# Kernel optimization log

Hardware: AMD Instinct MI355X
Metric: run time of the kernel (lower is better)

The kernel has to match this reference:

```python
import jax, jax.numpy as jnp
import numpy as np

T, D = 1024, 2048
H, KH, HD = 16, 4, 128
E, K, I = 8, 2, 2048
EPS = 1e-5
CAP = 30.0          # attn logit softcap and router logit softcap
BASE = 10000.0      # rope theta


def setup_inputs() -> dict:
    key = jax.random.key(0)
    ks = jax.random.split(key, 8)
    s = 0.02
    return {
        "positions": jnp.arange(T, dtype=jnp.int32),
        "hidden_states": jax.random.normal(ks[0], (T, D), jnp.float32),
        "w_qkv": jax.random.normal(ks[1], (D, (H + 2 * KH) * HD), jnp.float32) * s,
        "w_o": jax.random.normal(ks[2], (H * HD, D), jnp.float32) * s,
        "w_gate": jax.random.normal(ks[3], (D, E), jnp.float32) * s,
        "w_gate_up": jax.random.normal(ks[4], (E, D, 2 * I), jnp.float32) * s,
        "w_down": jax.random.normal(ks[5], (E, I, D), jnp.float32) * s,
        "w_pre_attn": 1.0 + 0.01 * jax.random.normal(ks[6], (D,), jnp.float32),
        "w_post_attn": jnp.ones((D,), jnp.float32),
        "w_pre_moe": 1.0 + 0.01 * jax.random.normal(ks[7], (D,), jnp.float32),
        "w_post_moe": jnp.ones((D,), jnp.float32),
    }


def rmsnorm(x, w):
    v = jnp.mean(jnp.square(x), axis=-1, keepdims=True)
    return x * jax.lax.rsqrt(v + EPS) * w


def rope_neox(pos, x):
    # x: [T, nH, HD]; full-head-dim neox-style rotation
    half = HD // 2
    inv = 1.0 / (BASE ** (jnp.arange(half, dtype=jnp.float32) * 2.0 / HD))
    f = pos.astype(jnp.float32)[:, None] * inv            # [T, half]
    cos, sin = jnp.cos(f)[:, None, :], jnp.sin(f)[:, None, :]
    x1, x2 = x[..., :half], x[..., half:]
    return jnp.concatenate([x1 * cos - x2 * sin, x2 * cos + x1 * sin], axis=-1)


def attention(pos, x, w_qkv, w_o):
    qkv = x @ w_qkv
    q, k, v = jnp.split(qkv, [H * HD, (H + KH) * HD], axis=-1)
    q = rope_neox(pos, q.reshape(T, H, HD))
    k = rope_neox(pos, k.reshape(T, KH, HD))
    v = v.reshape(T, KH, HD)
    rep = H // KH                                          # GQA repeat
    k = jnp.repeat(k, rep, axis=1)
    v = jnp.repeat(v, rep, axis=1)
    s = jnp.einsum('qhd,khd->hqk', q, k) * (HD ** -0.5)
    s = CAP * jnp.tanh(s / CAP)                            # tanh logit cap
    causal = pos[:, None] >= pos[None, :]
    s = jnp.where(causal[None], s, -1e30)
    p = jax.nn.softmax(s, axis=-1)
    o = jnp.einsum('hqk,khd->qhd', p, v).reshape(T, H * HD)
    return o @ w_o


def moe(x, w_gate, w_gate_up, w_down):
    logits = x @ w_gate
    logits = CAP * jnp.tanh(logits / CAP)                  # router softcap
    probs = jax.nn.softmax(logits, axis=-1)
    topv, topi = jax.lax.top_k(probs, K)                   # no renorm (Grok1)
    comb = jnp.zeros((T, E), probs.dtype).at[jnp.arange(T)[:, None], topi].set(topv)
    gu = jnp.einsum('td,edf->etf', x, w_gate_up)           # [E,T,2I]
    g, u = jnp.split(gu, 2, axis=-1)
    act = jax.nn.gelu(g, approximate=True) * u             # GeluAndMul(tanh)
    out_e = jnp.einsum('eti,eid->etd', act, w_down)        # [E,T,D]
    return jnp.einsum('etd,te->td', out_e, comb)


def reference(positions, hidden_states, w_qkv, w_o, w_gate, w_gate_up, w_down,
              w_pre_attn, w_post_attn, w_pre_moe, w_post_moe):
    resid = hidden_states
    h = rmsnorm(hidden_states, w_pre_attn)
    a = attention(positions, h, w_qkv, w_o)
    resid = resid + rmsnorm(a, w_post_attn)                # post_attn_norm + add
    h = rmsnorm(resid, w_pre_moe)
    m = moe(h, w_gate, w_gate_up, w_down)
    return resid + rmsnorm(m, w_post_moe)
```

## Files before the change

kernel.cpp:

```cpp
#include <hip/hip_runtime.h>

#define TT 1024
#define DD 2048
#define NH 16
#define NKV 4
#define HDIM 128
#define NE 8
#define NI 2048
#define EPSF 1e-5f
#define NP 4

typedef short bf16x8 __attribute__((ext_vector_type(8)));
typedef float f32x4 __attribute__((ext_vector_type(4)));

__device__ __forceinline__ unsigned short f2bf(float x) {
  unsigned u = __float_as_uint(x);
  u += 0x7FFFu + ((u >> 16) & 1u);
  return (unsigned short)(u >> 16);
}
__device__ __forceinline__ float bf2f(unsigned short h) {
  return __uint_as_float((unsigned)h << 16);
}
__device__ __forceinline__ void split2(float a, unsigned short& h,
                                       unsigned short& l) {
  h = f2bf(a);
  l = f2bf(a - bf2f(h));
}

__device__ __forceinline__ float wave_sum(float v) {
#pragma unroll
  for (int m = 32; m >= 1; m >>= 1) v += __shfl_xor(v, m, 64);
  return v;
}
__device__ __forceinline__ float wave_max(float v) {
#pragma unroll
  for (int m = 32; m >= 1; m >>= 1) v = fmaxf(v, __shfl_xor(v, m, 64));
  return v;
}

__device__ __forceinline__ int swz4(int r) { return (r ^ (r >> 2)) & 3; }
__device__ __forceinline__ int swz8(int r) { return (r ^ (r >> 3)) & 7; }

__device__ __forceinline__ void stage32(char* dst, const unsigned short* src,
                                        int rs, int tid) {
#pragma unroll
  for (int j = 0; j < 2; ++j) {
    int idx = tid + j * 256;
    int r = idx >> 2, c = idx & 3;
    bf16x8 v = *(const bf16x8*)(src + r * rs + c * 8);
    *(bf16x8*)(dst + r * 64 + ((c ^ swz4(r)) << 4)) = v;
  }
}
__device__ __forceinline__ void ld_frag(const char* base, int wrow, int l15,
                                        int lg, bf16x8* dst) {
#pragma unroll
  for (int i = 0; i < 4; ++i) {
    int row = wrow + i * 16 + l15;
    dst[i] = *(const bf16x8*)(base + row * 64 + ((lg ^ swz4(row)) << 4));
  }
}
__device__ __forceinline__ void mm16(const bf16x8* xa, const bf16x8* xb,
                                     f32x4 (*acc)[4]) {
#pragma unroll
  for (int mi = 0; mi < 4; ++mi)
#pragma unroll
    for (int ni = 0; ni < 4; ++ni)
      acc[mi][ni] = __builtin_amdgcn_mfma_f32_16x16x32_bf16(
          xa[mi], xb[ni], acc[mi][ni], 0, 0, 0);
}

template <int MODE>
__global__ __launch_bounds__(256) void pgemm3_k(
    const unsigned short* __restrict__ Ah, const unsigned short* __restrict__ Al,
    const unsigned short* __restrict__ Bh, const unsigned short* __restrict__ Bl,
    float* __restrict__ C, int Kh, int lda, int ldb, int ldc, long czs,
    float escale, float* __restrict__ SM, float* __restrict__ SS) {
  int z = blockIdx.z;
  int m0 = blockIdx.y * 128, n0 = blockIdx.x * 128;
  int k0 = 0, kend = Kh;
  if (MODE == 0) {
    k0 = z * Kh;
    kend = k0 + Kh;
    C += (long)z * czs;
  } else if (MODE == 1) {
    if (blockIdx.x > blockIdx.y) return;
    Ah += (long)z * TT * lda;
    Al += (long)z * TT * lda;
    Bh += (long)(z >> 2) * TT * ldb;
    Bl += (long)(z >> 2) * TT * ldb;
    C += (long)z * czs;
  } else {
    int head = z >> 2, ch = z & 3;
    int limit = (blockIdx.y + 1) * 128;
    k0 = ch * 256;
    if (k0 >= limit) return;
    kend = k0 + 256 < limit ? k0 + 256 : limit;
    Ah += (long)head * TT * lda;
    Al += (long)head * TT * lda;
    Bh += (long)(head >> 2) * HDIM * ldb;
    Bl += (long)(head >> 2) * HDIM * ldb;
    C += (long)ch * czs + head * HDIM;
  }

  __shared__ __align__(16) char lds[32768];
  int tid = threadIdx.x, lane = tid & 63, wid = tid >> 6;
  int wm = (wid >> 1) * 64, wn = (wid & 1) * 64;
  int l15 = lane & 15, lg = lane >> 4;

  f32x4 acc[4][4];
#pragma unroll
  for (int i = 0; i < 4; ++i)
#pragma unroll
    for (int j = 0; j < 4; ++j) acc[i][j] = {0.f, 0.f, 0.f, 0.f};

  for (int kt = k0; kt < kend; kt += 32) {
    __syncthreads();
    stage32(lds, Ah + (long)m0 * lda + kt, lda, tid);
    stage32(lds + 8192, Al + (long)m0 * lda + kt, lda, tid);
    stage32(lds + 16384, Bh + (long)n0 * ldb + kt, ldb, tid);
    stage32(lds + 24576, Bl + (long)n0 * ldb + kt, ldb, tid);
    __syncthreads();
    bf16x8 fah[4], fal[4], fbh[4], fbl[4];
    ld_frag(lds, wm, l15, lg, fah);
    ld_frag(lds + 16384, wn, l15, lg, fbh);
    mm16(fah, fbh, acc);
    ld_frag(lds + 24576, wn, l15, lg, fbl);
    mm16(fah, fbl, acc);
    ld_frag(lds + 8192, wm, l15, lg, fal);
    mm16(fal, fbh, acc);
  }

  if (MODE == 1) {
    int bx = blockIdx.x;
    bool diag = (bx == blockIdx.y);
    float vcap[4][4][4];
#pragma unroll
    for (int mi = 0; mi < 4; ++mi)
#pragma unroll
      for (int ni = 0; ni < 4; ++ni)
#pragma unroll
        for (int rr = 0; rr < 4; ++rr) {
          float v = acc[mi][ni][rr] * escale;
          vcap[mi][ni][rr] = 30.f * tanhf(v * (1.f / 30.f));
        }
#pragma unroll
    for (int mi = 0; mi < 4; ++mi)
#pragma unroll
      for (int ni = 0; ni < 4; ++ni)
#pragma unroll
        for (int rr = 0; rr < 4; ++rr) {
          int ml = m0 + wm + mi * 16 + lg * 4 + rr;
          int col = n0 + wn + ni * 16 + l15;
          C[(long)ml * ldc + col] = vcap[mi][ni][rr];
        }
    __syncthreads();
    float* wmx = (float*)lds;
    float* wsm = (float*)(lds + 1024);
    int ch = wid & 1;
#pragma unroll
    for (int mi = 0; mi < 4; ++mi)
#pragma unroll
      for (int rr = 0; rr < 4; ++rr) {
        int wr = wm + mi * 16 + lg * 4 + rr;
        int rowg = m0 + wr;
        float mx = -1e30f;
#pragma unroll
        for (int ni = 0; ni < 4; ++ni) {
          int colg = n0 + wn + ni * 16 + l15;
          if (!diag || colg <= rowg) mx = fmaxf(mx, vcap[mi][ni][rr]);
        }
#pragma unroll
        for (int mk = 1; mk <= 8; mk <<= 1)
          mx = fmaxf(mx, __shfl_xor(mx, mk, 64));
        if (l15 == 0) wmx[ch * 128 + wr] = mx;
      }
    __syncthreads();
#pragma unroll
    for (int mi = 0; mi < 4; ++mi)
#pragma unroll
      for (int rr = 0; rr < 4; ++rr) {
        int wr = wm + mi * 16 + lg * 4 + rr;
        int rowg = m0 + wr;
        float m2 = fmaxf(wmx[wr], wmx[128 + wr]);
        float s = 0.f;
#pragma unroll
        for (int ni = 0; ni < 4; ++ni) {
          int colg = n0 + wn + ni * 16 + l15;
          if (!diag || colg <= rowg) s += expf(vcap[mi][ni][rr] - m2);
        }
#pragma unroll
        for (int mk = 1; mk <= 8; mk <<= 1) s += __shfl_xor(s, mk, 64);
        if (l15 == 0) wsm[ch * 128 + wr] = s;
      }
    __syncthreads();
    if (tid < 128) {
      float m2 = fmaxf(wmx[tid], wmx[128 + tid]);
      float s = wsm[tid] + wsm[128 + tid];
      long so = ((long)z * 8 + bx) * TT + m0 + tid;
      SM[so] = m2;
      SS[so] = s;
    }
    return;
  }

#pragma unroll
  for (int mi = 0; mi < 4; ++mi)
#pragma unroll
    for (int ni = 0; ni < 4; ++ni)
#pragma unroll
      for (int rr = 0; rr < 4; ++rr) {
        int ml = m0 + wm + mi * 16 + lg * 4 + rr;
        int col = n0 + wn + ni * 16 + l15;
        C[(long)ml * ldc + col] = acc[mi][ni][rr];
      }
}

template <int AMODE, int EP, int KSL>
__global__ __launch_bounds__(256) void gemm_k(
    const unsigned short* __restrict__ A, const float* __restrict__ Bf,
    unsigned short* __restrict__ Cb, int N, int K, int lda, int ldb, int ldc,
    long bzs, long pzs, const int* __restrict__ cnt,
    const int* __restrict__ basep, const int* __restrict__ tok,
    const int* __restrict__ slotp, const float* __restrict__ wtp,
    unsigned short* __restrict__ slots_out) {
  int z = blockIdx.z;
  int e = z >> KSL, kp = z & ((1 << KSL) - 1);
  Bf += (long)e * bzs;
  int Me = cnt[e], be = basep[e];
  int m0 = blockIdx.y * 128, n0 = blockIdx.x * 128;
  if (m0 >= Me) return;
  int Kc = K >> KSL, kbeg = kp * Kc, klim = kbeg + Kc;

  __shared__ __align__(16) char lds[32768];
  const int BOFF = 16384;
  int tid = threadIdx.x, lane = tid & 63, wid = tid >> 6;
  int wm = (wid >> 1) * 64, wn = (wid & 1) * 64;
  int l15 = lane & 15, lg = lane >> 4;

  f32x4 acc[4][4];
#pragma unroll
  for (int i = 0; i < 4; ++i)
#pragma unroll
    for (int j = 0; j < 4; ++j) acc[i][j] = {0.f, 0.f, 0.f, 0.f};

  float breg[4][8];
  auto LOADB = [&](int kt) {
#pragma unroll
    for (int i = 0; i < 4; ++i) {
      int gidx = tid + i * 256;
      int n = gidx & 127, kc = gidx >> 7;
      const float* src = Bf + (long)(kt + kc * 8) * ldb + n0 + n;
#pragma unroll
      for (int u = 0; u < 8; ++u) breg[i][u] = src[(long)u * ldb];
    }
  };

  LOADB(kbeg);
  for (int kt = kbeg; kt < klim; kt += 64) {
    __syncthreads();
#pragma unroll
    for (int i = 0; i < 4; ++i) {
      int idx = tid + i * 256;
      int r = idx >> 3, c = idx & 7;
      int gm = m0 + r;
      bf16x8 v = {0, 0, 0, 0, 0, 0, 0, 0};
      bool ok = gm < Me;
      long arow;
      if (AMODE == 1)
        arow = ok ? (long)tok[e * TT + gm] : 0;
      else
        arow = (long)be + gm;
      if (ok) v = *(const bf16x8*)(A + arow * (long)lda + kt + c * 8);
      *(bf16x8*)(lds + r * 128 + ((c ^ swz8(r)) << 4)) = v;
    }
#pragma unroll
    for (int i = 0; i < 4; ++i) {
      int gidx = tid + i * 256;
      int n = gidx & 127, kc = gidx >> 7;
      bf16x8 v;
#pragma unroll
      for (int u = 0; u < 8; ++u)
        ((unsigned short*)&v)[u] = f2bf(breg[i][u]);
      *(bf16x8*)(lds + BOFF + n * 128 + ((kc ^ swz8(n)) << 4)) = v;
    }
    __syncthreads();
    if (kt + 64 < klim) LOADB(kt + 64);
#pragma unroll
    for (int s = 0; s < 2; ++s) {
      bf16x8 af[4], bfr[4];
      int slotk = s * 4 + lg;
#pragma unroll
      for (int mi = 0; mi < 4; ++mi) {
        int row = wm + mi * 16 + l15;
        af[mi] =
            *(const bf16x8*)(lds + row * 128 + ((slotk ^ swz8(row)) << 4));
      }
#pragma unroll
      for (int ni = 0; ni < 4; ++ni) {
        int row = wn + ni * 16 + l15;
        bfr[ni] = *(const bf16x8*)(lds + BOFF + row * 128 +
                                   ((slotk ^ swz8(row)) << 4));
      }
      mm16(af, bfr, acc);
    }
  }
#pragma unroll
  for (int mi = 0; mi < 4; ++mi)
#pragma unroll
    for (int ni = 0; ni < 4; ++ni)
#pragma unroll
      for (int rr = 0; rr < 4; ++rr) {
        int ml = m0 + wm + mi * 16 + lg * 4 + rr;
        int col = n0 + wn + ni * 16 + l15;
        float val = acc[mi][ni][rr];
        if (ml < Me) {
          if (EP == 0) {
            Cb[(long)kp * pzs + (long)(be + ml) * ldc + col] = f2bf(val);
          } else {
            int t = tok[e * TT + ml];
            int s = slotp[e * TT + ml];
            float w = wtp[e * TT + ml];
            slots_out[(long)kp * pzs + ((long)s * TT + t) * DD + col] =
                f2bf(val * w);
          }
        }
      }
}

__global__ __launch_bounds__(256) void tsplit_k(const float* __restrict__ W,
                                                unsigned short* __restrict__ Th,
                                                unsigned short* __restrict__ Tl,
                                                int K, int N) {
  __shared__ float lds[64 * 65];
  int n0 = blockIdx.x * 64, k0 = blockIdx.y * 64;
  int tid = threadIdx.x;
#pragma unroll
  for (int i = 0; i < 4; ++i) {
    int idx = tid + i * 256;
    int kr = idx >> 4, cg = idx & 15;
    float4 v = *(const float4*)(W + (long)(k0 + kr) * N + n0 + cg * 4);
    float* p = &lds[kr * 65 + cg * 4];
    p[0] = v.x; p[1] = v.y; p[2] = v.z; p[3] = v.w;
  }
  __syncthreads();
#pragma unroll
  for (int i = 0; i < 2; ++i) {
    int idx = tid + i * 256;
    int n = idx >> 3, kc = idx & 7;
    bf16x8 h8, l8;
#pragma unroll
    for (int u = 0; u < 8; ++u) {
      unsigned short hh, ll;
      split2(lds[(kc * 8 + u) * 65 + n], hh, ll);
      ((unsigned short*)&h8)[u] = hh;
      ((unsigned short*)&l8)[u] = ll;
    }
    long o = (long)(n0 + n) * K + k0 + kc * 8;
    *(bf16x8*)(Th + o) = h8;
    *(bf16x8*)(Tl + o) = l8;
  }
}

__global__ __launch_bounds__(256) void rms_pre_k(const float* __restrict__ x,
                                                 const float* __restrict__ w,
                                                 unsigned short* __restrict__ oh,
                                                 unsigned short* __restrict__ ol) {
  __shared__ float red[4];
  int t = blockIdx.x, tid = threadIdx.x;
  const float* xr = x + (long)t * DD;
  float xv[8];
  float ss = 0.f;
#pragma unroll
  for (int i = 0; i < 8; ++i) {
    float v = xr[tid + i * 256];
    xv[i] = v;
    ss += v * v;
  }
  ss = wave_sum(ss);
  if ((tid & 63) == 0) red[tid >> 6] = ss;
  __syncthreads();
  float r = rsqrtf((red[0] + red[1] + red[2] + red[3]) * (1.f / DD) + EPSF);
#pragma unroll
  for (int i = 0; i < 8; ++i) {
    int d = tid + i * 256;
    split2(xv[i] * r * w[d], oh[(long)t * DD + d], ol[(long)t * DD + d]);
  }
}

__global__ __launch_bounds__(256) void rope_qk_k(
    const int* __restrict__ pos, const float* __restrict__ qp,
    unsigned short* __restrict__ qh, unsigned short* __restrict__ ql,
    unsigned short* __restrict__ kh, unsigned short* __restrict__ kl) {
  __shared__ float cs[64], sn[64];
  int t = blockIdx.x, tid = threadIdx.x;
  float pf = (float)pos[t];
  if (tid < 64) {
    float inv = exp2f(-(float)tid * 0.20762050593046015f);
    float f = pf * inv;
    cs[tid] = cosf(f);
    sn[tid] = sinf(f);
  }
  __syncthreads();
  const float* row = qp + (long)t * 3072;
  const long PS = (long)TT * 3072;
#pragma unroll
  for (int i = 0; i < 4; ++i) {
    int idx = tid + i * 256;
    int h = idx >> 6, j = idx & 63;
    float x1 = 0.f, x2 = 0.f;
#pragma unroll
    for (int p = 0; p < NP; ++p) {
      x1 += row[p * PS + h * HDIM + j];
      x2 += row[p * PS + h * HDIM + 64 + j];
    }
    float c = cs[j], s = sn[j];
    long base = ((long)h * TT + t) * HDIM;
    split2(x1 * c - x2 * s, qh[base + j], ql[base + j]);
    split2(x2 * c + x1 * s, qh[base + 64 + j], ql[base + 64 + j]);
  }
  {
    int k2 = tid >> 6, j = tid & 63;
    float x1 = 0.f, x2 = 0.f;
#pragma unroll
    for (int p = 0; p < NP; ++p) {
      x1 += row[p * PS + 2048 + k2 * HDIM + j];
      x2 += row[p * PS + 2048 + k2 * HDIM + 64 + j];
    }
    float c = cs[j], s = sn[j];
    long base = ((long)k2 * TT + t) * HDIM;
    split2(x1 * c - x2 * s, kh[base + j], kl[base + j]);
    split2(x2 * c + x1 * s, kh[base + 64 + j], kl[base + 64 + j]);
  }
}

__global__ __launch_bounds__(256) void vtrans_k(const float* __restrict__ qp,
                                                unsigned short* __restrict__ Vh,
                                                unsigned short* __restrict__ Vl) {
  __shared__ float lds[64 * 129];
  int tb = blockIdx.x, kv = blockIdx.y;
  int t0 = tb * 128;
  int tid = threadIdx.x;
  const long PS = (long)TT * 3072;
#pragma unroll
  for (int dh = 0; dh < 2; ++dh) {
    if (dh) __syncthreads();
#pragma unroll
    for (int i = 0; i < 8; ++i) {
      int fidx = tid + i * 256;
      int t = fidx >> 4, dq = fidx & 15;
      long gi = (long)(t0 + t) * 3072 + 2560 + kv * HDIM + dh * 64 + dq * 4;
      float4 a = *(const float4*)(qp + gi);
#pragma unroll
      for (int p = 1; p < NP; ++p) {
        float4 b = *(const float4*)(qp + p * PS + gi);
        a.x += b.x; a.y += b.y; a.z += b.z; a.w += b.w;
      }
      lds[(dq * 4 + 0) * 129 + t] = a.x;
      lds[(dq * 4 + 1) * 129 + t] = a.y;
      lds[(dq * 4 + 2) * 129 + t] = a.z;
      lds[(dq * 4 + 3) * 129 + t] = a.w;
    }
    __syncthreads();
#pragma unroll
    for (int i = 0; i < 4; ++i) {
      int cidx = tid + i * 256;
      int d = cidx >> 4, tc = cidx & 15;
      bf16x8 h8, l8;
#pragma unroll
      for (int u = 0; u < 8; ++u) {
        unsigned short hh, ll;
        split2(lds[d * 129 + tc * 8 + u], hh, ll);
        ((unsigned short*)&h8)[u] = hh;
        ((unsigned short*)&l8)[u] = ll;
      }
      long o = ((long)kv * HDIM + dh * 64 + d) * TT + t0 + tc * 8;
      *(bf16x8*)(Vh + o) = h8;
      *(bf16x8*)(Vl + o) = l8;
    }
  }
}

__global__ __launch_bounds__(256) void softmax_k(const float* __restrict__ S,
                                                 const float* __restrict__ SM,
                                                 const float* __restrict__ SS,
                                                 unsigned short* __restrict__ Ph,
                                                 unsigned short* __restrict__ Pl) {
  int i = blockIdx.x, h = blockIdx.y, tid = threadIdx.x;
  int len = i + 1;
  int nt = (i >> 7) + 1;
  int wlimit = nt << 7;
  float m = -1e30f;
  for (int t = 0; t < nt; ++t)
    m = fmaxf(m, SM[((long)h * 8 + t) * TT + i]);
  float den = 0.f;
  for (int t = 0; t < nt; ++t) {
    long so = ((long)h * 8 + t) * TT + i;
    den += SS[so] * expf(SM[so] - m);
  }
  float inv = 1.f / den;
  const float* srow = S + ((long)h * TT + i) * TT;
  unsigned short* ph = Ph + ((long)h * TT + i) * TT;
  unsigned short* pl = Pl + ((long)h * TT + i) * TT;
  for (int j = tid; j < wlimit; j += 256) {
    float p = (j < len) ? expf(srow[j] - m) * inv : 0.f;
    unsigned short hh, ll;
    split2(p, hh, ll);
    ph[j] = hh;
    pl[j] = ll;
  }
}

__global__ __launch_bounds__(256) void obreduce_k(const float* __restrict__ obp,
                                                  unsigned short* __restrict__ oh,
                                                  unsigned short* __restrict__ ol) {
  int m = blockIdx.x, tid = threadIdx.x;
  int nv = ((m >> 7) >> 1) + 1;
#pragma unroll
  for (int i = 0; i < 8; ++i) {
    int d = tid + i * 256;
    float s = 0.f;
    for (int c = 0; c < nv; ++c) s += obp[(long)c * TT * DD + (long)m * DD + d];
    split2(s, oh[(long)m * DD + d], ol[(long)m * DD + d]);
  }
}

__global__ __launch_bounds__(256) void post_attn_k(
    const float* __restrict__ ap, const float* __restrict__ hidden,
    const float* __restrict__ w_post, const float* __restrict__ w_pre2,
    float* __restrict__ resid1, float* __restrict__ h2f,
    unsigned short* __restrict__ h2b) {
  __shared__ float red[4];
  int t = blockIdx.x, tid = threadIdx.x;
  const long PS = (long)TT * DD;
  float av[8];
  float ss = 0.f;
#pragma unroll
  for (int i = 0; i < 8; ++i) {
    long o = (long)t * DD + tid + i * 256;
    float v = 0.f;
#pragma unroll
    for (int p = 0; p < NP; ++p) v += ap[p * PS + o];
    av[i] = v;
    ss += v * v;
  }
  ss = wave_sum(ss);
  if ((tid & 63) == 0) red[tid >> 6] = ss;
  __syncthreads();
  float r1 = rsqrtf((red[0] + red[1] + red[2] + red[3]) * (1.f / DD) + EPSF);
  __syncthreads();
  float rv[8];
  float ss2 = 0.f;
#pragma unroll
  for (int i = 0; i < 8; ++i) {
    int d = tid + i * 256;
    float v = hidden[(long)t * DD + d] + av[i] * r1 * w_post[d];
    rv[i] = v;
    resid1[(long)t * DD + d] = v;
    ss2 += v * v;
  }
  ss2 = wave_sum(ss2);
  if ((tid & 63) == 0) red[tid >> 6] = ss2;
  __syncthreads();
  float r2 = rsqrtf((red[0] + red[1] + red[2] + red[3]) * (1.f / DD) + EPSF);
#pragma unroll
  for (int i = 0; i < 8; ++i) {
    int d = tid + i * 256;
    float hv = rv[i] * r2 * w_pre2[d];
    h2f[(long)t * DD + d] = hv;
    h2b[(long)t * DD + d] = f2bf(hv);
  }
}

__global__ __launch_bounds__(256) void gate_k(const float* __restrict__ h2f,
                                              const float* __restrict__ wg,
                                              int* cnt, int* tok, int* slotp,
                                              float* wtp) {
  __shared__ float red[4][8];
  int t = blockIdx.x, tid = threadIdx.x;
  float a[8] = {0, 0, 0, 0, 0, 0, 0, 0};
  const float* x = h2f + (long)t * DD;
  for (int d = tid; d < DD; d += 256) {
    float xv = x[d];
    const float* wr = wg + d * 8;
#pragma unroll
    for (int e = 0; e < 8; ++e) a[e] += xv * wr[e];
  }
#pragma unroll
  for (int e = 0; e < 8; ++e) a[e] = wave_sum(a[e]);
  if ((tid & 63) == 0) {
#pragma unroll
    for (int e = 0; e < 8; ++e) red[tid >> 6][e] = a[e];
  }
  __syncthreads();
  if (tid == 0) {
    float l[8], p[8];
    float m = -1e30f;
    for (int e = 0; e < 8; ++e) {
      float v = red[0][e] + red[1][e] + red[2][e] + red[3][e];
      v = 30.f * tanhf(v * (1.f / 30.f));
      l[e] = v;
      m = fmaxf(m, v);
    }
    float s = 0.f;
    for (int e = 0; e < 8; ++e) { p[e] = expf(l[e] - m); s += p[e]; }
    for (int e = 0; e < 8; ++e) p[e] /= s;
    int i1 = 0;
    for (int e = 1; e < 8; ++e) if (p[e] > p[i1]) i1 = e;
    int i2 = (i1 == 0) ? 1 : 0;
    for (int e = 0; e < 8; ++e) if (e != i1 && p[e] > p[i2]) i2 = e;
    int q1 = atomicAdd(&cnt[i1], 1);
    tok[i1 * TT + q1] = t; slotp[i1 * TT + q1] = 0; wtp[i1 * TT + q1] = p[i1];
    int q2 = atomicAdd(&cnt[i2], 1);
    tok[i2 * TT + q2] = t; slotp[i2 * TT + q2] = 1; wtp[i2 * TT + q2] = p[i2];
  }
}

__global__ void scan_k(const int* __restrict__ cnt, int* __restrict__ basep) {
  if (threadIdx.x == 0) {
    int s = 0;
    for (int e = 0; e < NE; ++e) { basep[e] = s; s += cnt[e]; }
    basep[NE] = s;
  }
}

__global__ __launch_bounds__(256) void act_k(const unsigned short* __restrict__ gu,
                                             unsigned short* __restrict__ actb) {
  long a = blockIdx.x;
  const long PS = (long)2 * TT * 2 * NI;
  const unsigned short* g0 = gu + a * (2 * NI);
  const unsigned short* g1 = g0 + PS;
  for (int i = threadIdx.x; i < NI; i += 256) {
    float gg = bf2f(g0[i]) + bf2f(g1[i]);
    float uu = bf2f(g0[i + NI]) + bf2f(g1[i + NI]);
    float c = gg + 0.044715f * gg * gg * gg;
    float act = 0.5f * gg * (1.f + tanhf(0.7978845608028654f * c));
    actb[a * NI + i] = f2bf(act * uu);
  }
}

__global__ __launch_bounds__(256) void final_k(
    const float* __restrict__ resid1, const unsigned short* __restrict__ slots,
    const float* __restrict__ w2, float* __restrict__ out) {
  __shared__ float red[4];
  int t = blockIdx.x, tid = threadIdx.x;
  const long PL = (long)TT * DD;
  float mv[8];
  float ss = 0.f;
#pragma unroll
  for (int i = 0; i < 8; ++i) {
    long o = (long)t * DD + tid + i * 256;
    float v = 0.f;
#pragma unroll
    for (int p = 0; p < 8; ++p) v += bf2f(slots[p * PL + o]);
    mv[i] = v;
    ss += v * v;
  }
  ss = wave_sum(ss);
  if ((tid & 63) == 0) red[tid >> 6] = ss;
  __syncthreads();
  float r = rsqrtf((red[0] + red[1] + red[2] + red[3]) * (1.f / DD) + EPSF);
#pragma unroll
  for (int i = 0; i < 8; ++i) {
    int d = tid + i * 256;
    out[(long)t * DD + d] = resid1[(long)t * DD + d] + mv[i] * r * w2[d];
  }
}

__global__ void sentinel_k(float* out) { out[threadIdx.x] = 12345.0f; }

extern "C" void kernel_launch(void* const* d_in, const int* in_sizes, int n_in,
                              void* d_out, int out_size, void* d_ws,
                              size_t ws_size, hipStream_t stream) {
  const int* pos = (const int*)d_in[0];
  const float* hidden = (const float*)d_in[1];
  const float* w_qkv = (const float*)d_in[2];
  const float* w_o = (const float*)d_in[3];
  const float* w_gate = (const float*)d_in[4];
  const float* w_gu = (const float*)d_in[5];
  const float* w_down = (const float*)d_in[6];
  const float* w_pre_attn = (const float*)d_in[7];
  const float* w_post_attn = (const float*)d_in[8];
  const float* w_pre_moe = (const float*)d_in[9];
  const float* w_post_moe = (const float*)d_in[10];
  float* out = (float*)d_out;

  char* ws = (char*)d_ws;
  size_t off = 0;
  auto alloc = [&](size_t bytes) {
    char* p = ws + off;
    off += (bytes + 255) & ~(size_t)255;
    return p;
  };
  typedef unsigned short u16;
  u16* h1h = (u16*)alloc((size_t)TT * DD * 2);
  u16* h1l = (u16*)alloc((size_t)TT * DD * 2);
  u16* wqkvTh = (u16*)alloc((size_t)3072 * DD * 2);
  u16* wqkvTl = (u16*)alloc((size_t)3072 * DD * 2);
  float* qkvp = (float*)alloc((size_t)NP * TT * 3072 * 4);
  u16* qh_ = (u16*)alloc((size_t)NH * TT * HDIM * 2);
  u16* ql_ = (u16*)alloc((size_t)NH * TT * HDIM * 2);
  u16* kh_ = (u16*)alloc((size_t)NKV * TT * HDIM * 2);
  u16* kl_ = (u16*)alloc((size_t)NKV * TT * HDIM * 2);
  u16* vth = (u16*)alloc((size_t)NKV * HDIM * TT * 2);
  u16* vtl = (u16*)alloc((size_t)NKV * HDIM * TT * 2);
  float* S = (float*)alloc((size_t)NH * TT * TT * 4);
  float* SMb = (float*)alloc((size_t)NH * 8 * TT * 4);
  float* SSb = (float*)alloc((size_t)NH * 8 * TT * 4);
  u16* Ph = (u16*)alloc((size_t)NH * TT * TT * 2);
  u16* Pl = (u16*)alloc((size_t)NH * TT * TT * 2);
  float* obp = (float*)alloc((size_t)4 * TT * DD * 4);
  u16* obh = (u16*)alloc((size_t)TT * DD * 2);
  u16* obl = (u16*)alloc((size_t)TT * DD * 2);
  u16* woTh = (u16*)alloc((size_t)DD * DD * 2);
  u16* woTl = (u16*)alloc((size_t)DD * DD * 2);
  float* attnp = (float*)alloc((size_t)NP * TT * DD * 4);
  float* resid1 = (float*)alloc((size_t)TT * DD * 4);
  float* h2f = (float*)alloc((size_t)TT * DD * 4);
  u16* h2b = (u16*)alloc((size_t)TT * DD * 2);
  int* cnt = (int*)alloc(NE * 4);
  int* basep = (int*)alloc((NE + 1) * 4);
  int* tok = (int*)alloc((size_t)NE * TT * 4);
  int* slotp = (int*)alloc((size_t)NE * TT * 4);
  float* wtp = (float*)alloc((size_t)NE * TT * 4);
  u16* gu = (u16*)alloc((size_t)2 * 2 * TT * 2 * NI * 2);
  u16* actb = (u16*)alloc((size_t)2 * TT * NI * 2);
  u16* slots = (u16*)alloc((size_t)4 * 2 * TT * DD * 2);

  if (off > ws_size) {
    sentinel_k<<<1, 256, 0, stream>>>(out);
    return;
  }

  hipMemsetAsync(cnt, 0, NE * 4, stream);
  dim3 blk(256);

  rms_pre_k<<<TT, blk, 0, stream>>>(hidden, w_pre_attn, h1h, h1l);
  tsplit_k<<<dim3(3072 / 64, DD / 64), blk, 0, stream>>>(w_qkv, wqkvTh, wqkvTl,
                                                         DD, 3072);
  tsplit_k<<<dim3(DD / 64, DD / 64), blk, 0, stream>>>(w_o, woTh, woTl, DD, DD);

  pgemm3_k<0><<<dim3(3072 / 128, TT / 128, NP), blk, 0, stream>>>(
      h1h, h1l, wqkvTh, wqkvTl, qkvp, DD / NP, DD, DD, 3072, (long)TT * 3072,
      0.f, nullptr, nullptr);

  rope_qk_k<<<TT, blk, 0, stream>>>(pos, qkvp, qh_, ql_, kh_, kl_);
  vtrans_k<<<dim3(8, NKV), blk, 0, stream>>>(qkvp, vth, vtl);

  pgemm3_k<1><<<dim3(TT / 128, TT / 128, NH), blk, 0, stream>>>(
      qh_, ql_, kh_, kl_, S, HDIM, HDIM, HDIM, TT, (long)TT * TT,
      0.08838834764831845f, SMb, SSb);

  softmax_k<<<dim3(TT, NH), blk, 0, stream>>>(S, SMb, SSb, Ph, Pl);

  pgemm3_k<2><<<dim3(1, TT / 128, NH * 4), blk, 0, stream>>>(
      Ph, Pl, vth, vtl, obp, 256, TT, TT, DD, (long)TT * DD, 0.f, nullptr,
      nullptr);
  obreduce_k<<<TT, blk, 0, stream>>>(obp, obh, obl);

  pgemm3_k<0><<<dim3(DD / 128, TT / 128, NP), blk, 0, stream>>>(
      obh, obl, woTh, woTl, attnp, DD / NP, DD, DD, DD, (long)TT * DD, 0.f,
      nullptr, nullptr);

  post_attn_k<<<TT, blk, 0, stream>>>(attnp, hidden, w_post_attn, w_pre_moe,
                                      resid1, h2f, h2b);
  gate_k<<<TT, blk, 0, stream>>>(h2f, w_gate, cnt, tok, slotp, wtp);
  scan_k<<<1, 64, 0, stream>>>(cnt, basep);

  gemm_k<1, 0, 1><<<dim3(2 * NI / 128, TT / 128, NE * 2), blk, 0, stream>>>(
      h2b, w_gu, gu, 2 * NI, DD, DD, 2 * NI, 2 * NI, (long)DD * 2 * NI,
      (long)2 * TT * 2 * NI, cnt, basep, tok, nullptr, nullptr, nullptr);

  act_k<<<2 * TT, blk, 0, stream>>>(gu, actb);

  gemm_k<2, 3, 2><<<dim3(DD / 128, TT / 128, NE * 4), blk, 0, stream>>>(
      actb, w_down, nullptr, DD, NI, NI, DD, DD, (long)NI * DD,
      (long)2 * TT * DD, cnt, basep, tok, slotp, wtp, slots);

  final_k<<<TT, blk, 0, stream>>>(resid1, slots, w_post_moe, out);
}
```

Baseline: 525.8 us.

## Stage split-bf16 GEMM tiles via global_load_lds with pre-swizzled producer layouts

The split-precision GEMM now stages tiles with direct global-to-LDS loads instead of going through registers. To keep LDS reads bank-conflict free, every producer kernel (transposes, rmsnorm, rope, softmax, V transpose, o-reduce) writes its bf16 outputs in a pre-swizzled column order. Separately, the MoE gemm drops its register prefetch of B and loads B inline, and the down projection uses a 2-way instead of 4-way K split, so final_k sums fewer slots. This reduces VGPR staging and partial-sum traffic, at the cost of losing B prefetch overlap and some parallelism in the down GEMM.

```diff
diff --git a/kernel.cpp b/kernel.cpp
--- a/kernel.cpp
+++ b/kernel.cpp
@@ -41,14 +41,22 @@
 __device__ __forceinline__ int swz4(int r) { return (r ^ (r >> 2)) & 3; }
 __device__ __forceinline__ int swz8(int r) { return (r ^ (r >> 3)) & 7; }
 
-__device__ __forceinline__ void stage32(char* dst, const unsigned short* src,
-                                        int rs, int tid) {
+__device__ __forceinline__ int swzoff(int row, int k) {
+  return (k & ~31) | ((((k >> 3) & 3) ^ swz4(row & 15)) << 3) | (k & 7);
+}
+
+__device__ __forceinline__ void stage_gll(const unsigned short* src, int ld,
+                                          char* ldsbase, int wid, int lane) {
 #pragma unroll
   for (int j = 0; j < 2; ++j) {
-    int idx = tid + j * 256;
+    int idx = (wid * 2 + j) * 64 + lane;
     int r = idx >> 2, c = idx & 3;
-    bf16x8 v = *(const bf16x8*)(src + r * rs + c * 8);
-    *(bf16x8*)(dst + r * 64 + ((c ^ swz4(r)) << 4)) = v;
+    const unsigned short* g = src + (long)r * ld + c * 8;
+    __builtin_amdgcn_global_load_lds(
+        (const __attribute__((address_space(1))) unsigned int*)g,
+        (__attribute__((address_space(3))) unsigned int*)(ldsbase +
+                                                         (wid * 2 + j) * 1024),
+        16, 0, 0);
   }
 }
 __device__ __forceinline__ void ld_frag(const char* base, int wrow, int l15,
@@ -115,10 +123,10 @@
 
   for (int kt = k0; kt < kend; kt += 32) {
     __syncthreads();
-    stage32(lds, Ah + (long)m0 * lda + kt, lda, tid);
-    stage32(lds + 8192, Al + (long)m0 * lda + kt, lda, tid);
-    stage32(lds + 16384, Bh + (long)n0 * ldb + kt, ldb, tid);
-    stage32(lds + 24576, Bl + (long)n0 * ldb + kt, ldb, tid);
+    stage_gll(Ah + (long)m0 * lda + kt, lda, lds, wid, lane);
+    stage_gll(Al + (long)m0 * lda + kt, lda, lds + 8192, wid, lane);
+    stage_gll(Bh + (long)n0 * ldb + kt, ldb, lds + 16384, wid, lane);
+    stage_gll(Bl + (long)n0 * ldb + kt, ldb, lds + 24576, wid, lane);
     __syncthreads();
     bf16x8 fah[4], fal[4], fbh[4], fbl[4];
     ld_frag(lds, wm, l15, lg, fah);
@@ -215,7 +223,7 @@
       }
 }
 
-template <int AMODE, int EP, int KSL>
+template <int AMODE, int EP>
 __global__ __launch_bounds__(256) void gemm_k(
     const unsigned short* __restrict__ A, const float* __restrict__ Bf,
     unsigned short* __restrict__ Cb, int N, int K, int lda, int ldb, int ldc,
@@ -224,12 +232,12 @@
     const int* __restrict__ slotp, const float* __restrict__ wtp,
     unsigned short* __restrict__ slots_out) {
   int z = blockIdx.z;
-  int e = z >> KSL, kp = z & ((1 << KSL) - 1);
+  int e = z >> 1, kp = z & 1;
   Bf += (long)e * bzs;
   int Me = cnt[e], be = basep[e];
   int m0 = blockIdx.y * 128, n0 = blockIdx.x * 128;
   if (m0 >= Me) return;
-  int Kc = K >> KSL, kbeg = kp * Kc, klim = kbeg + Kc;
+  int Kc = K >> 1, kbeg = kp * Kc, klim = kbeg + Kc;
 
   __shared__ __align__(16) char lds[32768];
   const int BOFF = 16384;
@@ -243,19 +251,6 @@
 #pragma unroll
     for (int j = 0; j < 4; ++j) acc[i][j] = {0.f, 0.f, 0.f, 0.f};
 
-  float breg[4][8];
-  auto LOADB = [&](int kt) {
-#pragma unroll
-    for (int i = 0; i < 4; ++i) {
-      int gidx = tid + i * 256;
-      int n = gidx & 127, kc = gidx >> 7;
-      const float* src = Bf + (long)(kt + kc * 8) * ldb + n0 + n;
-#pragma unroll
-      for (int u = 0; u < 8; ++u) breg[i][u] = src[(long)u * ldb];
-    }
-  };
-
-  LOADB(kbeg);
   for (int kt = kbeg; kt < klim; kt += 64) {
     __syncthreads();
 #pragma unroll
@@ -277,14 +272,14 @@
     for (int i = 0; i < 4; ++i) {
       int gidx = tid + i * 256;
       int n = gidx & 127, kc = gidx >> 7;
+      const float* src = Bf + (long)(kt + kc * 8) * ldb + n0 + n;
       bf16x8 v;
 #pragma unroll
       for (int u = 0; u < 8; ++u)
-        ((unsigned short*)&v)[u] = f2bf(breg[i][u]);
+        ((unsigned short*)&v)[u] = f2bf(src[(long)u * ldb]);
       *(bf16x8*)(lds + BOFF + n * 128 + ((kc ^ swz8(n)) << 4)) = v;
     }
     __syncthreads();
-    if (kt + 64 < klim) LOADB(kt + 64);
 #pragma unroll
     for (int s = 0; s < 2; ++s) {
       bf16x8 af[4], bfr[4];
@@ -355,7 +350,8 @@
       ((unsigned short*)&h8)[u] = hh;
       ((unsigned short*)&l8)[u] = ll;
     }
-    long o = (long)(n0 + n) * K + k0 + kc * 8;
+    int row = n0 + n;
+    long o = (long)row * K + swzoff(row, k0 + kc * 8);
     *(bf16x8*)(Th + o) = h8;
     *(bf16x8*)(Tl + o) = l8;
   }
@@ -383,7 +379,8 @@
 #pragma unroll
   for (int i = 0; i < 8; ++i) {
     int d = tid + i * 256;
-    split2(xv[i] * r * w[d], oh[(long)t * DD + d], ol[(long)t * DD + d]);
+    int ds = swzoff(t, d);
+    split2(xv[i] * r * w[d], oh[(long)t * DD + ds], ol[(long)t * DD + ds]);
   }
 }
 
@@ -415,8 +412,9 @@
     }
     float c = cs[j], s = sn[j];
     long base = ((long)h * TT + t) * HDIM;
-    split2(x1 * c - x2 * s, qh[base + j], ql[base + j]);
-    split2(x2 * c + x1 * s, qh[base + 64 + j], ql[base + 64 + j]);
+    split2(x1 * c - x2 * s, qh[base + swzoff(t, j)], ql[base + swzoff(t, j)]);
+    split2(x2 * c + x1 * s, qh[base + swzoff(t, 64 + j)],
+           ql[base + swzoff(t, 64 + j)]);
   }
   {
     int k2 = tid >> 6, j = tid & 63;
@@ -428,8 +426,9 @@
     }
     float c = cs[j], s = sn[j];
     long base = ((long)k2 * TT + t) * HDIM;
-    split2(x1 * c - x2 * s, kh[base + j], kl[base + j]);
-    split2(x2 * c + x1 * s, kh[base + 64 + j], kl[base + 64 + j]);
+    split2(x1 * c - x2 * s, kh[base + swzoff(t, j)], kl[base + swzoff(t, j)]);
+    split2(x2 * c + x1 * s, kh[base + swzoff(t, 64 + j)],
+           kl[base + swzoff(t, 64 + j)]);
   }
 }
 
@@ -473,7 +472,8 @@
         ((unsigned short*)&h8)[u] = hh;
         ((unsigned short*)&l8)[u] = ll;
       }
-      long o = ((long)kv * HDIM + dh * 64 + d) * TT + t0 + tc * 8;
+      int rowd = dh * 64 + d;
+      long o = ((long)kv * HDIM + rowd) * TT + swzoff(rowd, t0 + tc * 8);
       *(bf16x8*)(Vh + o) = h8;
       *(bf16x8*)(Vl + o) = l8;
     }
@@ -505,8 +505,9 @@
     float p = (j < len) ? expf(srow[j] - m) * inv : 0.f;
     unsigned short hh, ll;
     split2(p, hh, ll);
-    ph[j] = hh;
-    pl[j] = ll;
+    int js = swzoff(i, j);
+    ph[js] = hh;
+    pl[js] = ll;
   }
 }
 
@@ -520,7 +521,8 @@
     int d = tid + i * 256;
     float s = 0.f;
     for (int c = 0; c < nv; ++c) s += obp[(long)c * TT * DD + (long)m * DD + d];
-    split2(s, oh[(long)m * DD + d], ol[(long)m * DD + d]);
+    int ds = swzoff(m, d);
+    split2(s, oh[(long)m * DD + ds], ol[(long)m * DD + ds]);
   }
 }
 
@@ -649,9 +651,8 @@
 #pragma unroll
   for (int i = 0; i < 8; ++i) {
     long o = (long)t * DD + tid + i * 256;
-    float v = 0.f;
-#pragma unroll
-    for (int p = 0; p < 8; ++p) v += bf2f(slots[p * PL + o]);
+    float v = bf2f(slots[o]) + bf2f(slots[PL + o]) + bf2f(slots[2 * PL + o]) +
+              bf2f(slots[3 * PL + o]);
     mv[i] = v;
     ss += v * v;
   }
@@ -724,7 +725,7 @@
   float* wtp = (float*)alloc((size_t)NE * TT * 4);
   u16* gu = (u16*)alloc((size_t)2 * 2 * TT * 2 * NI * 2);
   u16* actb = (u16*)alloc((size_t)2 * TT * NI * 2);
-  u16* slots = (u16*)alloc((size_t)4 * 2 * TT * DD * 2);
+  u16* slots = (u16*)alloc((size_t)2 * 2 * TT * DD * 2);
 
   if (off > ws_size) {
     sentinel_k<<<1, 256, 0, stream>>>(out);
@@ -766,13 +767,13 @@
   gate_k<<<TT, blk, 0, stream>>>(h2f, w_gate, cnt, tok, slotp, wtp);
   scan_k<<<1, 64, 0, stream>>>(cnt, basep);
 
-  gemm_k<1, 0, 1><<<dim3(2 * NI / 128, TT / 128, NE * 2), blk, 0, stream>>>(
+  gemm_k<1, 0><<<dim3(2 * NI / 128, TT / 128, NE * 2), blk, 0, stream>>>(
       h2b, w_gu, gu, 2 * NI, DD, DD, 2 * NI, 2 * NI, (long)DD * 2 * NI,
       (long)2 * TT * 2 * NI, cnt, basep, tok, nullptr, nullptr, nullptr);
 
   act_k<<<2 * TT, blk, 0, stream>>>(gu, actb);
 
-  gemm_k<2, 3, 2><<<dim3(DD / 128, TT / 128, NE * 4), blk, 0, stream>>>(
+  gemm_k<2, 3><<<dim3(DD / 128, TT / 128, NE * 2), blk, 0, stream>>>(
       actb, w_down, nullptr, DD, NI, NI, DD, DD, (long)NI * DD,
       (long)2 * TT * DD, cnt, basep, tok, slotp, wtp, slots);
 
```

Result: faster. 493.9 us (-6.1%).
